# Kernel optimization log

Measured on AMD Instinct MI355X. Metric: run time of the kernel, lower is better.

Reference implementation:

```python
import jax, jax.numpy as jnp
import numpy as np

N = 150000   # nodes
E = 600000   # edges
F_IN = 32    # node features
H = 128      # hidden_channels == MLP_neurons
G = 2048     # graphs in batch


def setup_inputs() -> dict:
    key = jax.random.key(0)
    ks = iter(jax.random.split(key, 40))
    inp = {}
    inp['x'] = jax.random.normal(next(ks), (N, F_IN), dtype=jnp.float32)
    inp['edge_index'] = jax.random.randint(next(ks), (2, E), 0, N)
    inp['batch'] = jnp.sort(jax.random.randint(next(ks), (N,), 0, G))
    # GINConv MLPs: Linear(in,H) ReLU Linear(H,H) ReLU Linear(H,H)
    for i, f_in in enumerate([F_IN, H, H]):
        s1 = 1.0 / np.sqrt(f_in)
        s2 = 1.0 / np.sqrt(H)
        inp[f'c{i}_w1'] = jax.random.uniform(next(ks), (f_in, H), minval=-s1, maxval=s1)
        inp[f'c{i}_b1'] = jnp.zeros((H,), jnp.float32)
        inp[f'c{i}_w2'] = jax.random.uniform(next(ks), (H, H), minval=-s2, maxval=s2)
        inp[f'c{i}_b2'] = jnp.zeros((H,), jnp.float32)
        inp[f'c{i}_w3'] = jax.random.uniform(next(ks), (H, H), minval=-s2, maxval=s2)
        inp[f'c{i}_b3'] = jnp.zeros((H,), jnp.float32)
    s = 1.0 / np.sqrt(H)
    inp['fc0_w'] = jax.random.uniform(next(ks), (H, H), minval=-s, maxval=s)
    inp['fc0_b'] = jnp.zeros((H,), jnp.float32)
    inp['fc1_w'] = jax.random.uniform(next(ks), (H, H), minval=-s, maxval=s)
    inp['fc1_b'] = jnp.zeros((H,), jnp.float32)
    inp['out_w'] = jax.random.uniform(next(ks), (H, 2), minval=-s, maxval=s)
    inp['out_b'] = jnp.zeros((2,), jnp.float32)
    return inp


def _gin_layer(x, edge_index, w1, b1, w2, b2, w3, b3):
    # GINConv with eps=0: h = MLP(x + sum_{j in N(i)} x_j)
    agg = jax.ops.segment_sum(x[edge_index[0]], edge_index[1], num_segments=N)
    h = x + agg
    h = jax.nn.relu(h @ w1 + b1)
    h = jax.nn.relu(h @ w2 + b2)
    h = h @ w3 + b3
    return jax.nn.relu(h)  # outer .relu() in forward


def reference(x, edge_index, batch,
              c0_w1, c0_b1, c0_w2, c0_b2, c0_w3, c0_b3,
              c1_w1, c1_b1, c1_w2, c1_b2, c1_w3, c1_b3,
              c2_w1, c2_b1, c2_w2, c2_b2, c2_w3, c2_b3,
              fc0_w, fc0_b, fc1_w, fc1_b, out_w, out_b):
    h = _gin_layer(x, edge_index, c0_w1, c0_b1, c0_w2, c0_b2, c0_w3, c0_b3)
    h = _gin_layer(h, edge_index, c1_w1, c1_b1, c1_w2, c1_b2, c1_w3, c1_b3)
    h = _gin_layer(h, edge_index, c2_w1, c2_b1, c2_w2, c2_b2, c2_w3, c2_b3)
    # global_mean_pool over graph ids
    sums = jax.ops.segment_sum(h, batch, num_segments=G)            # [G,H]
    cnts = jax.ops.segment_sum(jnp.ones((N,), h.dtype), batch, num_segments=G)
    g = sums / jnp.maximum(cnts, 1.0)[:, None]
    # classifier head (dropout is identity at inference)
    g = jax.nn.relu(g @ fc0_w + fc0_b)
    g = jax.nn.relu(g @ fc1_w + fc1_b)
    return g @ out_w + out_b  # [G,2]
```

## Files before the change

kernel.cpp:

```cpp
#include <hip/hip_runtime.h>
#include <hip/hip_bf16.h>

#define NN 150000
#define EE 600000
#define F_IN 32
#define HD 128
#define GG 2048
#define CAP 28
#define NP 150016

typedef __attribute__((ext_vector_type(8))) short bf16x8;
typedef __attribute__((ext_vector_type(4))) float f32x4;

__device__ inline void split_bf16(float v, unsigned short& hi, unsigned short& lo) {
    __hip_bfloat16 h = __float2bfloat16(v);
    float hv = __bfloat162float(h);
    __hip_bfloat16 l = __float2bfloat16(v - hv);
    hi = *reinterpret_cast<unsigned short*>(&h);
    lo = *reinterpret_cast<unsigned short*>(&l);
}
__device__ inline unsigned short bf16_hi(float v) {
    __hip_bfloat16 h = __float2bfloat16(v);
    return *reinterpret_cast<unsigned short*>(&h);
}
__device__ inline unsigned short bf16_lo(float v) {
    __hip_bfloat16 h = __float2bfloat16(v);
    float hv = __bfloat162float(h);
    __hip_bfloat16 l = __float2bfloat16(v - hv);
    return *reinterpret_cast<unsigned short*>(&l);
}
__device__ inline float bf2f(unsigned short u) {
    union { unsigned int i; float f; } c;
    c.i = ((unsigned int)u) << 16;
    return c.f;
}

__global__ void init_zero(int* __restrict__ cnt_node, int* __restrict__ cntg,
                          float* __restrict__ pooled) {
    int i = blockIdx.x * blockDim.x + threadIdx.x;
    if (i < NN) cnt_node[i] = 0;
    if (i < GG) cntg[i] = 0;
    if (i < GG * HD) pooled[i] = 0.f;
}

__global__ void build_graph(const int* __restrict__ ei, const int* __restrict__ batch,
                            int* __restrict__ cnt_node, int* __restrict__ cntg,
                            int* __restrict__ bucket) {
    int e = blockIdx.x * blockDim.x + threadIdx.x;
    if (e < NN) atomicAdd(&cntg[batch[e]], 1);
    if (e >= EE) return;
    int src = ei[e];
    int dst = ei[EE + e];
    int slot = atomicAdd(&cnt_node[dst], 1);
    if (slot < CAP) bucket[dst * CAP + slot] = src;
}

struct PrepDesc { const float* src; unsigned short* dhi; unsigned short* dlo; int K; };
struct PrepArgs { PrepDesc d[9]; };

__global__ void prep_weights(PrepArgs pa) {
    PrepDesc de = pa.d[blockIdx.y];
    int total = de.K * HD;
    int KS = de.K >> 5;
    for (int idx = blockIdx.x * blockDim.x + threadIdx.x; idx < total;
         idx += gridDim.x * blockDim.x) {
        int k = idx / HD, h = idx - (idx / HD) * HD;
        unsigned short hi, lo;
        split_bf16(de.src[idx], hi, lo);
        int nt = h >> 4, m = h & 15;
        int ks = k >> 5, quad = (k >> 3) & 3, e = k & 7;
        int lane = quad * 16 + m;
        int pidx = ((nt * KS + ks) * 64 + lane) * 8 + e;
        de.dhi[pidx] = hi;
        de.dlo[pidx] = lo;
    }
}

template <int K_IN, bool BF16IN, bool POOL>
__launch_bounds__(256, 3)
__global__ void gin_layer(const void* __restrict__ hin_,
                          const int* __restrict__ cnt_node,
                          const int* __restrict__ bucket,
                          const unsigned short* __restrict__ w1h, const unsigned short* __restrict__ w1l,
                          const float* __restrict__ b1,
                          const unsigned short* __restrict__ w2h, const unsigned short* __restrict__ w2l,
                          const float* __restrict__ b2,
                          const unsigned short* __restrict__ w3h, const unsigned short* __restrict__ w3l,
                          const float* __restrict__ b3,
                          unsigned short* __restrict__ out,
                          const int* __restrict__ batch,
                          float* __restrict__ pooled) {
    constexpr int KS1 = K_IN / 32;
    constexpr int UN = BF16IN ? 4 : (KS1 == 1 ? 8 : 2);
    __shared__ unsigned short sh[4][32][HD + 8];

    const int wave = threadIdx.x >> 6;
    const int lane = threadIdx.x & 63;
    const int m = lane & 15;
    const int quad = lane >> 4;
    const int nodeBase = blockIdx.x * 128 + wave * 32;

    const float* hf = (const float*)hin_;
    const unsigned short* hb = (const unsigned short*)hin_;

    bf16x8 ah[2][KS1], al[2][KS1];
#pragma unroll
    for (int s = 0; s < 2; s++) {
        int node = nodeBase + s * 16 + m;
        node = node < NN ? node : NN - 1;
        float ag[KS1][8];
        if (BF16IN) {
            const unsigned short* rs = hb + (size_t)node * K_IN + quad * 8;
#pragma unroll
            for (int ks = 0; ks < KS1; ks++) {
                bf16x8 v = *(const bf16x8*)(rs + ks * 32);
#pragma unroll
                for (int e = 0; e < 8; e++) ag[ks][e] = bf2f((unsigned short)v[e]);
            }
        } else {
            const float* rs = hf + (size_t)node * K_IN + quad * 8;
#pragma unroll
            for (int ks = 0; ks < KS1; ks++) {
                float4 v0 = *(const float4*)(rs + ks * 32);
                float4 v1 = *(const float4*)(rs + ks * 32 + 4);
                ag[ks][0] = v0.x; ag[ks][1] = v0.y; ag[ks][2] = v0.z; ag[ks][3] = v0.w;
                ag[ks][4] = v1.x; ag[ks][5] = v1.y; ag[ks][6] = v1.z; ag[ks][7] = v1.w;
            }
        }
        int cnt = cnt_node[node];
        cnt = cnt < CAP ? cnt : CAP;
        const int* b = bucket + (size_t)node * CAP;
        int i = 0;
        if (BF16IN) {
            for (; i + UN <= cnt; i += UN) {
                bf16x8 v[UN][KS1];
#pragma unroll
                for (int j = 0; j < UN; j++) {
                    const unsigned short* r = hb + (size_t)b[i + j] * K_IN + quad * 8;
#pragma unroll
                    for (int ks = 0; ks < KS1; ks++)
                        v[j][ks] = *(const bf16x8*)(r + ks * 32);
                }
#pragma unroll
                for (int ks = 0; ks < KS1; ks++)
#pragma unroll
                    for (int e = 0; e < 8; e++) {
                        float t01 = bf2f((unsigned short)v[0][ks][e]) +
                                    bf2f((unsigned short)v[1][ks][e]);
                        float t23 = bf2f((unsigned short)v[2][ks][e]) +
                                    bf2f((unsigned short)v[3][ks][e]);
                        ag[ks][e] += t01 + t23;
                    }
            }
            for (; i < cnt; i++) {
                const unsigned short* r = hb + (size_t)b[i] * K_IN + quad * 8;
#pragma unroll
                for (int ks = 0; ks < KS1; ks++) {
                    bf16x8 v = *(const bf16x8*)(r + ks * 32);
#pragma unroll
                    for (int e = 0; e < 8; e++) ag[ks][e] += bf2f((unsigned short)v[e]);
                }
            }
        } else {
            for (; i + UN <= cnt; i += UN) {
                float4 v0[UN][KS1], v1[UN][KS1];
#pragma unroll
                for (int j = 0; j < UN; j++) {
                    const float* r = hf + (size_t)b[i + j] * K_IN + quad * 8;
#pragma unroll
                    for (int ks = 0; ks < KS1; ks++) {
                        v0[j][ks] = *(const float4*)(r + ks * 32);
                        v1[j][ks] = *(const float4*)(r + ks * 32 + 4);
                    }
                }
#pragma unroll
                for (int ks = 0; ks < KS1; ks++) {
                    float t0[8], t1[8];
#pragma unroll
                    for (int e = 0; e < 4; e++) {
                        float aA = (&v0[0][ks].x)[e], aB = (&v0[1][ks].x)[e];
                        float aC = (&v0[2][ks].x)[e], aD = (&v0[3][ks].x)[e];
                        float s01 = aA + aB, s23 = aC + aD;
                        if (UN == 8) {
                            float aE = (&v0[4][ks].x)[e], aF = (&v0[5][ks].x)[e];
                            float aG = (&v0[6][ks].x)[e], aH = (&v0[7][ks].x)[e];
                            s01 += aE + aF;
                            s23 += aG + aH;
                        }
                        t0[e] = s01 + s23;
                    }
#pragma unroll
                    for (int e = 0; e < 4; e++) {
                        float aA = (&v1[0][ks].x)[e], aB = (&v1[1][ks].x)[e];
                        float aC = (&v1[2][ks].x)[e], aD = (&v1[3][ks].x)[e];
                        float s01 = aA + aB, s23 = aC + aD;
                        if (UN == 8) {
                            float aE = (&v1[4][ks].x)[e], aF = (&v1[5][ks].x)[e];
                            float aG = (&v1[6][ks].x)[e], aH = (&v1[7][ks].x)[e];
                            s01 += aE + aF;
                            s23 += aG + aH;
                        }
                        t1[e] = s01 + s23;
                    }
#pragma unroll
                    for (int e = 0; e < 4; e++) {
                        ag[ks][e] += t0[e];
                        ag[ks][e + 4] += t1[e];
                    }
                }
            }
            for (; i < cnt; i++) {
                const float* r = hf + (size_t)b[i] * K_IN + quad * 8;
#pragma unroll
                for (int ks = 0; ks < KS1; ks++) {
                    float4 v0 = *(const float4*)(r + ks * 32);
                    float4 v1 = *(const float4*)(r + ks * 32 + 4);
                    ag[ks][0] += v0.x; ag[ks][1] += v0.y; ag[ks][2] += v0.z; ag[ks][3] += v0.w;
                    ag[ks][4] += v1.x; ag[ks][5] += v1.y; ag[ks][6] += v1.z; ag[ks][7] += v1.w;
                }
            }
        }
#pragma unroll
        for (int ks = 0; ks < KS1; ks++) {
            bf16x8 vh, vl;
#pragma unroll
            for (int e = 0; e < 8; e++) {
                unsigned short hi, lo;
                split_bf16(ag[ks][e], hi, lo);
                vh[e] = (short)hi;
                vl[e] = (short)lo;
            }
            ah[s][ks] = vh;
            al[s][ks] = vl;
        }
    }

    f32x4 acc[2][8];

#pragma unroll
    for (int nt = 0; nt < 8; nt++) {
        bf16x8 bh[KS1], bl[KS1];
#pragma unroll
        for (int ks = 0; ks < KS1; ks++) {
            bh[ks] = *(const bf16x8*)(w1h + ((nt * KS1 + ks) * 64 + lane) * 8);
            bl[ks] = *(const bf16x8*)(w1l + ((nt * KS1 + ks) * 64 + lane) * 8);
        }
        f32x4 c0 = {0.f, 0.f, 0.f, 0.f};
        f32x4 c1 = {0.f, 0.f, 0.f, 0.f};
#pragma unroll
        for (int ks = 0; ks < KS1; ks++) {
            c0 = __builtin_amdgcn_mfma_f32_16x16x32_bf16(ah[0][ks], bh[ks], c0, 0, 0, 0);
            c1 = __builtin_amdgcn_mfma_f32_16x16x32_bf16(ah[1][ks], bh[ks], c1, 0, 0, 0);
            c0 = __builtin_amdgcn_mfma_f32_16x16x32_bf16(al[0][ks], bh[ks], c0, 0, 0, 0);
            c1 = __builtin_amdgcn_mfma_f32_16x16x32_bf16(al[1][ks], bh[ks], c1, 0, 0, 0);
            c0 = __builtin_amdgcn_mfma_f32_16x16x32_bf16(ah[0][ks], bl[ks], c0, 0, 0, 0);
            c1 = __builtin_amdgcn_mfma_f32_16x16x32_bf16(ah[1][ks], bl[ks], c1, 0, 0, 0);
        }
        acc[0][nt] = c0;
        acc[1][nt] = c1;
    }

    bf16x8 a2h[2][4], a2l[2][4];
#pragma unroll
    for (int s = 0; s < 2; s++)
#pragma unroll
        for (int nt = 0; nt < 8; nt++) {
            float bj = b1[nt * 16 + m];
#pragma unroll
            for (int r = 0; r < 4; r++)
                sh[wave][s * 16 + quad * 4 + r][nt * 16 + m] =
                    bf16_hi(fmaxf(acc[s][nt][r] + bj, 0.f));
        }
#pragma unroll
    for (int s = 0; s < 2; s++)
#pragma unroll
        for (int ks = 0; ks < 4; ks++)
            a2h[s][ks] = *(const bf16x8*)&sh[wave][s * 16 + m][ks * 32 + quad * 8];
#pragma unroll
    for (int s = 0; s < 2; s++)
#pragma unroll
        for (int nt = 0; nt < 8; nt++) {
            float bj = b1[nt * 16 + m];
#pragma unroll
            for (int r = 0; r < 4; r++)
                sh[wave][s * 16 + quad * 4 + r][nt * 16 + m] =
                    bf16_lo(fmaxf(acc[s][nt][r] + bj, 0.f));
        }
#pragma unroll
    for (int s = 0; s < 2; s++)
#pragma unroll
        for (int ks = 0; ks < 4; ks++)
            a2l[s][ks] = *(const bf16x8*)&sh[wave][s * 16 + m][ks * 32 + quad * 8];

#pragma unroll
    for (int nt = 0; nt < 8; nt++) {
        bf16x8 bh[4], bl[4];
#pragma unroll
        for (int ks = 0; ks < 4; ks++) {
            bh[ks] = *(const bf16x8*)(w2h + ((nt * 4 + ks) * 64 + lane) * 8);
            bl[ks] = *(const bf16x8*)(w2l + ((nt * 4 + ks) * 64 + lane) * 8);
        }
        f32x4 c0 = {0.f, 0.f, 0.f, 0.f};
        f32x4 c1 = {0.f, 0.f, 0.f, 0.f};
#pragma unroll
        for (int ks = 0; ks < 4; ks++) {
            c0 = __builtin_amdgcn_mfma_f32_16x16x32_bf16(a2h[0][ks], bh[ks], c0, 0, 0, 0);
            c1 = __builtin_amdgcn_mfma_f32_16x16x32_bf16(a2h[1][ks], bh[ks], c1, 0, 0, 0);
            c0 = __builtin_amdgcn_mfma_f32_16x16x32_bf16(a2l[0][ks], bh[ks], c0, 0, 0, 0);
            c1 = __builtin_amdgcn_mfma_f32_16x16x32_bf16(a2l[1][ks], bh[ks], c1, 0, 0, 0);
            c0 = __builtin_amdgcn_mfma_f32_16x16x32_bf16(a2h[0][ks], bl[ks], c0, 0, 0, 0);
            c1 = __builtin_amdgcn_mfma_f32_16x16x32_bf16(a2h[1][ks], bl[ks], c1, 0, 0, 0);
        }
        acc[0][nt] = c0;
        acc[1][nt] = c1;
    }

#pragma unroll
    for (int s = 0; s < 2; s++)
#pragma unroll
        for (int nt = 0; nt < 8; nt++) {
            float bj = b2[nt * 16 + m];
#pragma unroll
            for (int r = 0; r < 4; r++)
                sh[wave][s * 16 + quad * 4 + r][nt * 16 + m] =
                    bf16_hi(fmaxf(acc[s][nt][r] + bj, 0.f));
        }
#pragma unroll
    for (int s = 0; s < 2; s++)
#pragma unroll
        for (int ks = 0; ks < 4; ks++)
            a2h[s][ks] = *(const bf16x8*)&sh[wave][s * 16 + m][ks * 32 + quad * 8];
#pragma unroll
    for (int s = 0; s < 2; s++)
#pragma unroll
        for (int nt = 0; nt < 8; nt++) {
            float bj = b2[nt * 16 + m];
#pragma unroll
            for (int r = 0; r < 4; r++)
                sh[wave][s * 16 + quad * 4 + r][nt * 16 + m] =
                    bf16_lo(fmaxf(acc[s][nt][r] + bj, 0.f));
        }
#pragma unroll
    for (int s = 0; s < 2; s++)
#pragma unroll
        for (int ks = 0; ks < 4; ks++)
            a2l[s][ks] = *(const bf16x8*)&sh[wave][s * 16 + m][ks * 32 + quad * 8];

#pragma unroll
    for (int nt = 0; nt < 8; nt++) {
        bf16x8 bh[4], bl[4];
#pragma unroll
        for (int ks = 0; ks < 4; ks++) {
            bh[ks] = *(const bf16x8*)(w3h + ((nt * 4 + ks) * 64 + lane) * 8);
            bl[ks] = *(const bf16x8*)(w3l + ((nt * 4 + ks) * 64 + lane) * 8);
        }
        f32x4 c0 = {0.f, 0.f, 0.f, 0.f};
        f32x4 c1 = {0.f, 0.f, 0.f, 0.f};
#pragma unroll
        for (int ks = 0; ks < 4; ks++) {
            c0 = __builtin_amdgcn_mfma_f32_16x16x32_bf16(a2h[0][ks], bh[ks], c0, 0, 0, 0);
            c1 = __builtin_amdgcn_mfma_f32_16x16x32_bf16(a2h[1][ks], bh[ks], c1, 0, 0, 0);
            c0 = __builtin_amdgcn_mfma_f32_16x16x32_bf16(a2l[0][ks], bh[ks], c0, 0, 0, 0);
            c1 = __builtin_amdgcn_mfma_f32_16x16x32_bf16(a2l[1][ks], bh[ks], c1, 0, 0, 0);
            c0 = __builtin_amdgcn_mfma_f32_16x16x32_bf16(a2h[0][ks], bl[ks], c0, 0, 0, 0);
            c1 = __builtin_amdgcn_mfma_f32_16x16x32_bf16(a2h[1][ks], bl[ks], c1, 0, 0, 0);
        }
        acc[0][nt] = c0;
        acc[1][nt] = c1;
    }

    if (POOL) {
        float* shf = (float*)&sh[wave][0][0];
#pragma unroll
        for (int h = 0; h < 2; h++) {
#pragma unroll
            for (int nt = 0; nt < 8; nt++) {
                float bj = b3[nt * 16 + m];
#pragma unroll
                for (int r = 0; r < 4; r++)
                    shf[(quad * 4 + r) * 132 + nt * 16 + m] =
                        fmaxf(acc[h][nt][r] + bj, 0.f);
            }
            int c0 = lane * 2;
            float run0 = 0.f, run1 = 0.f;
            int gp = -1;
            for (int rrow = 0; rrow < 16; rrow++) {
                int node = nodeBase + h * 16 + rrow;
                if (node >= NN) break;
                int g = batch[node];
                float2 xv = *(const float2*)&shf[rrow * 132 + c0];
                if (g != gp) {
                    if (gp >= 0) {
                        atomicAdd(&pooled[(size_t)gp * HD + c0 + 0], run0);
                        atomicAdd(&pooled[(size_t)gp * HD + c0 + 1], run1);
                    }
                    run0 = xv.x; run1 = xv.y; gp = g;
                } else {
                    run0 += xv.x; run1 += xv.y;
                }
            }
            if (gp >= 0) {
                atomicAdd(&pooled[(size_t)gp * HD + c0 + 0], run0);
                atomicAdd(&pooled[(size_t)gp * HD + c0 + 1], run1);
            }
        }
    } else {
#pragma unroll
        for (int s = 0; s < 2; s++)
#pragma unroll
            for (int nt = 0; nt < 8; nt++) {
                float bj = b3[nt * 16 + m];
#pragma unroll
                for (int r = 0; r < 4; r++)
                    sh[wave][s * 16 + quad * 4 + r][nt * 16 + m] =
                        bf16_hi(fmaxf(acc[s][nt][r] + bj, 0.f));
            }
#pragma unroll
        for (int io = 0; io < 8; io++) {
            int row32 = io * 4 + quad;
            int col = m * 8;
            int n2 = nodeBase + row32;
            bf16x8 v = *(const bf16x8*)&sh[wave][row32][col];
            if (n2 < NN) *(bf16x8*)&out[(size_t)n2 * HD + col] = v;
        }
    }
}

__launch_bounds__(128)
__global__ void head(const float* __restrict__ pooled, const int* __restrict__ cntg,
                     const float* __restrict__ fc0_w, const float* __restrict__ fc0_b,
                     const float* __restrict__ fc1_w, const float* __restrict__ fc1_b,
                     const float* __restrict__ out_w, const float* __restrict__ out_b,
                     float* __restrict__ out) {
    int g = blockIdx.x;
    int j = threadIdx.x;
    __shared__ float s0[HD];
    __shared__ float s1[HD];
    int c = cntg[g];
    float cf = (float)(c > 1 ? c : 1);
    s0[j] = pooled[(size_t)g * HD + j] / cf;
    __syncthreads();

    float acc = fc0_b[j];
    for (int k = 0; k < HD; k += 4) {
        float4 hv = *(const float4*)&s0[k];
        acc = fmaf(hv.x, fc0_w[(k + 0) * HD + j], acc);
        acc = fmaf(hv.y, fc0_w[(k + 1) * HD + j], acc);
        acc = fmaf(hv.z, fc0_w[(k + 2) * HD + j], acc);
        acc = fmaf(hv.w, fc0_w[(k + 3) * HD + j], acc);
    }
    s1[j] = fmaxf(acc, 0.0f);
    __syncthreads();

    acc = fc1_b[j];
    for (int k = 0; k < HD; k += 4) {
        float4 hv = *(const float4*)&s1[k];
        acc = fmaf(hv.x, fc1_w[(k + 0) * HD + j], acc);
        acc = fmaf(hv.y, fc1_w[(k + 1) * HD + j], acc);
        acc = fmaf(hv.z, fc1_w[(k + 2) * HD + j], acc);
        acc = fmaf(hv.w, fc1_w[(k + 3) * HD + j], acc);
    }
    float v = fmaxf(acc, 0.0f);

    float p0 = v * out_w[j * 2 + 0];
    float p1 = v * out_w[j * 2 + 1];
    __syncthreads();
    s0[j] = p0;
    s1[j] = p1;
    __syncthreads();
    for (int off = 64; off >= 1; off >>= 1) {
        if (j < off) {
            s0[j] += s0[j + off];
            s1[j] += s1[j + off];
        }
        __syncthreads();
    }
    if (j == 0) {
        out[(size_t)g * 2 + 0] = s0[0] + out_b[0];
        out[(size_t)g * 2 + 1] = s1[0] + out_b[1];
    }
}

extern "C" void kernel_launch(void* const* d_in, const int* in_sizes, int n_in,
                              void* d_out, int out_size, void* d_ws, size_t ws_size,
                              hipStream_t stream) {
    const float* x     = (const float*)d_in[0];
    const int*   ei    = (const int*)d_in[1];
    const int*   batch = (const int*)d_in[2];
    const float* cw[3][6];
    for (int i = 0; i < 3; i++)
        for (int k = 0; k < 6; k++) cw[i][k] = (const float*)d_in[3 + 6 * i + k];
    const float* fc0_w = (const float*)d_in[21];
    const float* fc0_b = (const float*)d_in[22];
    const float* fc1_w = (const float*)d_in[23];
    const float* fc1_b = (const float*)d_in[24];
    const float* out_w = (const float*)d_in[25];
    const float* out_b = (const float*)d_in[26];
    float* out = (float*)d_out;

    char* ws = (char*)d_ws;
    size_t off = 0;
    auto carve = [&](size_t bytes) {
        void* p = ws + off;
        off += (bytes + 255) & ~(size_t)255;
        return p;
    };
    int*   cnt_node = (int*)carve((size_t)NN * 4);
    int*   cntg     = (int*)carve((size_t)GG * 4);
    float* pooled   = (float*)carve((size_t)GG * HD * 4);
    int*   bucket   = (int*)carve((size_t)NN * CAP * 4);
    unsigned short* hA = (unsigned short*)carve((size_t)NP * HD * 2);
    unsigned short* hB = (unsigned short*)carve((size_t)NP * HD * 2);
    unsigned short* wHi[9];
    unsigned short* wLo[9];
    int wK[9] = {F_IN, HD, HD, HD, HD, HD, HD, HD, HD};
    for (int i = 0; i < 9; i++) {
        wHi[i] = (unsigned short*)carve((size_t)wK[i] * HD * 2);
        wLo[i] = (unsigned short*)carve((size_t)wK[i] * HD * 2);
    }
    (void)ws_size;

    init_zero<<<(GG * HD + 255) / 256, 256, 0, stream>>>(cnt_node, cntg, pooled);
    build_graph<<<(EE + 255) / 256, 256, 0, stream>>>(ei, batch, cnt_node, cntg, bucket);

    PrepArgs pa;
    for (int l = 0; l < 3; l++)
        for (int s = 0; s < 3; s++) {
            int i = l * 3 + s;
            pa.d[i].src = cw[l][2 * s];
            pa.d[i].dhi = wHi[i];
            pa.d[i].dlo = wLo[i];
            pa.d[i].K = wK[i];
        }
    prep_weights<<<dim3(16, 9), 256, 0, stream>>>(pa);

    const int blocks = NP / 128;

    gin_layer<F_IN, false, false><<<blocks, 256, 0, stream>>>(x, cnt_node, bucket,
        wHi[0], wLo[0], cw[0][1], wHi[1], wLo[1], cw[0][3], wHi[2], wLo[2], cw[0][5],
        hA, batch, pooled);
    gin_layer<HD, true, false><<<blocks, 256, 0, stream>>>(hA, cnt_node, bucket,
        wHi[3], wLo[3], cw[1][1], wHi[4], wLo[4], cw[1][3], wHi[5], wLo[5], cw[1][5],
        hB, batch, pooled);
    gin_layer<HD, true, true><<<blocks, 256, 0, stream>>>(hB, cnt_node, bucket,
        wHi[6], wLo[6], cw[2][1], wHi[7], wLo[7], cw[2][3], wHi[8], wLo[8], cw[2][5],
        nullptr, batch, pooled);

    head<<<GG, 128, 0, stream>>>(pooled, cntg, fc0_w, fc0_b, fc1_w, fc1_b, out_w, out_b, out);
}
```

Baseline: 549.8 us.

## Add cooperative coalesced neighbor gather through LDS for layer-two aggregation

Adds a COOP path where each wave stages its 16 nodes' neighbor indices in shared memory, then has all 64 lanes load full 256-byte neighbor rows coalesced (4 rows per pass) into LDS, double-buffered in registers, before each lane sums its slice. Only the second layer uses it. CAP grows from 28 to 32 so index rows align and the bucket buffer is padded. The trade-off is that every wave iterates to the max degree in its group, plus extra LDS traffic and shared memory that may lower occupancy. The fp32 path accumulation is also tidied.

```diff
diff --git a/kernel.cpp b/kernel.cpp
--- a/kernel.cpp
+++ b/kernel.cpp
@@ -6,7 +6,7 @@
 #define F_IN 32
 #define HD 128
 #define GG 2048
-#define CAP 28
+#define CAP 32
 #define NP 150016
 
 typedef __attribute__((ext_vector_type(8))) short bf16x8;
@@ -76,7 +76,7 @@
     }
 }
 
-template <int K_IN, bool BF16IN, bool POOL>
+template <int K_IN, bool BF16IN, bool COOP, bool POOL>
 __launch_bounds__(256, 3)
 __global__ void gin_layer(const void* __restrict__ hin_,
                           const int* __restrict__ cnt_node,
@@ -93,6 +93,7 @@
     constexpr int KS1 = K_IN / 32;
     constexpr int UN = BF16IN ? 4 : (KS1 == 1 ? 8 : 2);
     __shared__ unsigned short sh[4][32][HD + 8];
+    __shared__ int shIdx[4][16][CAP];
 
     const int wave = threadIdx.x >> 6;
     const int lane = threadIdx.x & 63;
@@ -129,9 +130,60 @@
         }
         int cnt = cnt_node[node];
         cnt = cnt < CAP ? cnt : CAP;
-        const int* b = bucket + (size_t)node * CAP;
-        int i = 0;
-        if (BF16IN) {
+
+        if constexpr (COOP && BF16IN) {
+            {
+                const int* bsrc = bucket + (size_t)(nodeBase + s * 16) * CAP;
+#pragma unroll
+                for (int it = 0; it < 8; it++) {
+                    int fi = it * 64 + lane;
+                    int id = bsrc[fi];
+                    id = ((unsigned)id < (unsigned)NN) ? id : 0;
+                    shIdx[wave][fi >> 5][fi & 31] = id;
+                }
+            }
+            int kmax = cnt;
+#pragma unroll
+            for (int off = 1; off < 64; off <<= 1) {
+                int o = __shfl_xor(kmax, off);
+                kmax = kmax > o ? kmax : o;
+            }
+            const int rl = lane >> 4;
+            const int ch = (lane & 15) * 8;
+            bf16x8 vA[4], vB[4];
+            if (kmax > 0) {
+#pragma unroll
+                for (int j = 0; j < 4; j++) {
+                    int nb = shIdx[wave][4 * j + rl][0];
+                    vA[j] = *(const bf16x8*)(hb + (size_t)nb * K_IN + ch);
+                }
+            }
+            for (int k = 0; k < kmax; k++) {
+                bf16x8* vc = (k & 1) ? vB : vA;
+                bf16x8* vn = (k & 1) ? vA : vB;
+                if (k + 1 < kmax) {
+#pragma unroll
+                    for (int j = 0; j < 4; j++) {
+                        int nb = shIdx[wave][4 * j + rl][k + 1];
+                        vn[j] = *(const bf16x8*)(hb + (size_t)nb * K_IN + ch);
+                    }
+                }
+#pragma unroll
+                for (int j = 0; j < 4; j++)
+                    *(bf16x8*)&sh[wave][4 * j + rl][ch] = vc[j];
+                if (k < cnt) {
+#pragma unroll
+                    for (int ks = 0; ks < KS1; ks++) {
+                        bf16x8 v = *(const bf16x8*)&sh[wave][m][ks * 32 + quad * 8];
+#pragma unroll
+                        for (int e = 0; e < 8; e++)
+                            ag[ks][e] += bf2f((unsigned short)v[e]);
+                    }
+                }
+            }
+        } else if (BF16IN) {
+            const int* b = bucket + (size_t)node * CAP;
+            int i = 0;
             for (; i + UN <= cnt; i += UN) {
                 bf16x8 v[UN][KS1];
 #pragma unroll
@@ -162,6 +214,8 @@
                 }
             }
         } else {
+            const int* b = bucket + (size_t)node * CAP;
+            int i = 0;
             for (; i + UN <= cnt; i += UN) {
                 float4 v0[UN][KS1], v1[UN][KS1];
 #pragma unroll
@@ -175,37 +229,25 @@
                 }
 #pragma unroll
                 for (int ks = 0; ks < KS1; ks++) {
-                    float t0[8], t1[8];
 #pragma unroll
                     for (int e = 0; e < 4; e++) {
-                        float aA = (&v0[0][ks].x)[e], aB = (&v0[1][ks].x)[e];
-                        float aC = (&v0[2][ks].x)[e], aD = (&v0[3][ks].x)[e];
-                        float s01 = aA + aB, s23 = aC + aD;
+                        float s01 = (&v0[0][ks].x)[e] + (&v0[1][ks].x)[e];
+                        float s23 = (&v0[2][ks].x)[e] + (&v0[3][ks].x)[e];
                         if (UN == 8) {
-                            float aE = (&v0[4][ks].x)[e], aF = (&v0[5][ks].x)[e];
-                            float aG = (&v0[6][ks].x)[e], aH = (&v0[7][ks].x)[e];
-                            s01 += aE + aF;
-                            s23 += aG + aH;
+                            s01 += (&v0[4][ks].x)[e] + (&v0[5][ks].x)[e];
+                            s23 += (&v0[6][ks].x)[e] + (&v0[7][ks].x)[e];
                         }
-                        t0[e] = s01 + s23;
+                        ag[ks][e] += s01 + s23;
                     }
 #pragma unroll
                     for (int e = 0; e < 4; e++) {
-                        float aA = (&v1[0][ks].x)[e], aB = (&v1[1][ks].x)[e];
-                        float aC = (&v1[2][ks].x)[e], aD = (&v1[3][ks].x)[e];
-                        float s01 = aA + aB, s23 = aC + aD;
+                        float s01 = (&v1[0][ks].x)[e] + (&v1[1][ks].x)[e];
+                        float s23 = (&v1[2][ks].x)[e] + (&v1[3][ks].x)[e];
                         if (UN == 8) {
-                            float aE = (&v1[4][ks].x)[e], aF = (&v1[5][ks].x)[e];
-                            float aG = (&v1[6][ks].x)[e], aH = (&v1[7][ks].x)[e];
-                            s01 += aE + aF;
-                            s23 += aG + aH;
+                            s01 += (&v1[4][ks].x)[e] + (&v1[5][ks].x)[e];
+                            s23 += (&v1[6][ks].x)[e] + (&v1[7][ks].x)[e];
                         }
-                        t1[e] = s01 + s23;
-                    }
-#pragma unroll
-                    for (int e = 0; e < 4; e++) {
-                        ag[ks][e] += t0[e];
-                        ag[ks][e + 4] += t1[e];
+                        ag[ks][e + 4] += s01 + s23;
                     }
                 }
             }
@@ -508,7 +550,7 @@
     int*   cnt_node = (int*)carve((size_t)NN * 4);
     int*   cntg     = (int*)carve((size_t)GG * 4);
     float* pooled   = (float*)carve((size_t)GG * HD * 4);
-    int*   bucket   = (int*)carve((size_t)NN * CAP * 4);
+    int*   bucket   = (int*)carve((size_t)(NP + 16) * CAP * 4);
     unsigned short* hA = (unsigned short*)carve((size_t)NP * HD * 2);
     unsigned short* hB = (unsigned short*)carve((size_t)NP * HD * 2);
     unsigned short* wHi[9];
@@ -536,13 +578,13 @@
 
     const int blocks = NP / 128;
 
-    gin_layer<F_IN, false, false><<<blocks, 256, 0, stream>>>(x, cnt_node, bucket,
+    gin_layer<F_IN, false, false, false><<<blocks, 256, 0, stream>>>(x, cnt_node, bucket,
         wHi[0], wLo[0], cw[0][1], wHi[1], wLo[1], cw[0][3], wHi[2], wLo[2], cw[0][5],
         hA, batch, pooled);
-    gin_layer<HD, true, false><<<blocks, 256, 0, stream>>>(hA, cnt_node, bucket,
+    gin_layer<HD, true, true, false><<<blocks, 256, 0, stream>>>(hA, cnt_node, bucket,
         wHi[3], wLo[3], cw[1][1], wHi[4], wLo[4], cw[1][3], wHi[5], wLo[5], cw[1][5],
         hB, batch, pooled);
-    gin_layer<HD, true, true><<<blocks, 256, 0, stream>>>(hB, cnt_node, bucket,
+    gin_layer<HD, true, false, true><<<blocks, 256, 0, stream>>>(hB, cnt_node, bucket,
         wHi[6], wLo[6], cw[2][1], wHi[7], wLo[7], cw[2][3], wHi[8], wLo[8], cw[2][5],
         nullptr, batch, pooled);
 
```

Measured after the change: 548.3 us. About the same (-0.3%).
